# Performance work log

Hardware: AMD Instinct MI355X
Metric: run time of the kernel (lower is better)

Reference implementation:

```python
import jax, jax.numpy as jnp
import numpy as np

N_WIRES = 10
DIM = 1 << N_WIRES          # 1024 amplitudes per token state
HIDDEN = 64                 # number of Pauli-Z-string measurements (= hidden_dim)
B, T = 8, 2048

# ops[k] = Z-string on qubits in bitmask (k+1): <psi|Z_mask|psi> = sum_i |psi_i|^2 * (-1)^popcount(i & mask)
_masks = np.arange(1, HIDDEN + 1, dtype=np.int64)
_ii = np.arange(DIM, dtype=np.int64)
_pc = (((_ii[None, :] & _masks[:, None])[..., None] >> np.arange(N_WIRES)) & 1).sum(-1)
SIGNS = jnp.asarray(1.0 - 2.0 * (_pc % 2), dtype=jnp.float32)   # (HIDDEN, DIM)

CNOT = jnp.array([[1, 0, 0, 0], [0, 1, 0, 0], [0, 0, 0, 1], [0, 0, 1, 0]], dtype=jnp.complex64)

def _rx(theta):
    c = jnp.cos(theta / 2).astype(jnp.complex64)
    s = jnp.sin(theta / 2).astype(jnp.complex64)
    return jnp.stack([jnp.stack([c, -1j * s]), jnp.stack([-1j * s, c])])

def _ry(theta):
    c = jnp.cos(theta / 2).astype(jnp.complex64)
    s = jnp.sin(theta / 2).astype(jnp.complex64)
    return jnp.stack([jnp.stack([c, -s]), jnp.stack([s, c])])

def _apply_1q(psi, g, j, n):
    # qubit 0 is the most-significant bit of the state index (matches expand_operator bit order)
    left, right = 1 << j, 1 << (n - 1 - j)
    p = psi.reshape(-1, left, 2, right)
    p = jnp.einsum('ab,mlbr->mlar', g, p)
    return p.reshape(-1, 1 << n)

def _apply_2q(psi, g, q0, q1, n):
    p = psi.reshape((-1,) + (2,) * n)
    p = jnp.moveaxis(p, (1 + q0, 1 + q1), (1, 2))
    p = jnp.einsum('abcd,mcd...->mab...', g.reshape(2, 2, 2, 2), p)
    p = jnp.moveaxis(p, (1, 2), (1 + q0, 1 + q1))
    return p.reshape(-1, 1 << n)

def _forward(x, rx0, ry0, ry1):
    n, dim = N_WIRES, DIM
    Bb, Tt, C = x.shape
    M = Bb * Tt
    # AmplitudeEncoder: zero-pad features to 2^n and L2-normalize
    psi = jnp.zeros((M, dim), jnp.complex64).at[:, :C].set(x.reshape(M, C).astype(jnp.complex64))
    nrm = jnp.sqrt(jnp.sum(psi.real**2 + psi.imag**2, axis=1, keepdims=True))
    psi = psi / nrm.astype(jnp.complex64)
    # U_total = (prod_j RY1_j) (prod_j CNOT_{j,(j+1)%n}) (prod_j RY0_j RX0_j), applied to psi.
    # Applying the gate sequence directly to the state == matmul with the expanded U_total.
    rx0_d = jax.lax.stop_gradient(rx0)  # original detaches RX params via .item()
    for j in range(n):
        psi = _apply_1q(psi, _rx(rx0_d[j]), j, n)
        psi = _apply_1q(psi, _ry(ry0[j]), j, n)
    for j in range(n):
        psi = _apply_2q(psi, CNOT, j, (j + 1) % n, n)
    for j in range(n):
        psi = _apply_1q(psi, _ry(ry1[j]), j, n)
    probs = psi.real**2 + psi.imag**2            # (M, DIM)
    out = probs @ SIGNS.T                        # (M, HIDDEN) Pauli-Z-string expectations
    return out.reshape(Bb, Tt, HIDDEN).astype(jnp.float32)

def setup_inputs():
    key = jax.random.key(0)
    k1, k2, k3, k4 = jax.random.split(key, 4)
    two_pi = 2.0 * float(np.pi)
    return {
        'x': jax.random.normal(k1, (B, T, HIDDEN), dtype=jnp.float32),
        'rx0': jax.random.uniform(k2, (N_WIRES,), dtype=jnp.float32, maxval=two_pi),
        'ry0': jax.random.uniform(k3, (N_WIRES,), dtype=jnp.float32, maxval=two_pi),
        'ry1': jax.random.uniform(k4, (N_WIRES,), dtype=jnp.float32, maxval=two_pi),
    }

def reference(x, rx0, ry0, ry1):
    return _forward(x, rx0, ry0, ry1)
```

## Files before the change

kernel.cpp:

```cpp
#include <hip/hip_runtime.h>

typedef __bf16 v8bf __attribute__((ext_vector_type(8)));
typedef float v4f __attribute__((ext_vector_type(4)));
typedef unsigned short u16x8 __attribute__((ext_vector_type(8)));

__device__ __forceinline__ unsigned short f2bf(float f) {
    unsigned int u = __float_as_uint(f);
    u += 0x7FFFu + ((u >> 16) & 1u);
    return (unsigned short)(u >> 16);
}

__device__ __forceinline__ v8bf ld_bf8(const unsigned short* p) {
    u16x8 r = *(const u16x8*)p;
    return __builtin_bit_cast(v8bf, r);
}

__global__ __launch_bounds__(256) void build_V(
        const float* __restrict__ rx0, const float* __restrict__ ry0,
        const float* __restrict__ ry1,
        unsigned short* __restrict__ Vre, unsigned short* __restrict__ Vim)
{
    __shared__ float sre[1024];
    __shared__ float sim[1024];
    const int c = blockIdx.x;
    const int t = threadIdx.x;

    for (int k = 0; k < 4; ++k) {
        int i = t + k * 256;
        sre[i] = (i == c) ? 1.0f : 0.0f;
        sim[i] = 0.0f;
    }
    __syncthreads();

    for (int j = 0; j < 10; ++j) {
        float hx = 0.5f * rx0[j], hy = 0.5f * ry0[j];
        float cx = cosf(hx), sx = sinf(hx);
        float cy = cosf(hy), sy = sinf(hy);
        float g00r =  cy * cx, g00i =  sy * sx;
        float g01r = -sy * cx, g01i = -cy * sx;
        float g10r =  sy * cx, g10i = -cy * sx;
        float g11r =  cy * cx, g11i = -sy * sx;
        int p = 9 - j;
        int lowmask = (1 << p) - 1;
        #pragma unroll
        for (int it = 0; it < 2; ++it) {
            int idx = t + it * 256;
            int a = ((idx >> p) << (p + 1)) | (idx & lowmask);
            int b = a | (1 << p);
            float ar = sre[a], ai = sim[a], br = sre[b], bi = sim[b];
            sre[a] = g00r*ar - g00i*ai + g01r*br - g01i*bi;
            sim[a] = g00r*ai + g00i*ar + g01r*bi + g01i*br;
            sre[b] = g10r*ar - g10i*ai + g11r*br - g11i*bi;
            sim[b] = g10r*ai + g10i*ar + g11r*bi + g11i*br;
        }
        __syncthreads();
    }
    for (int j = 0; j < 10; ++j) {
        int pc = 9 - j;
        int pt = 9 - ((j + 1) % 10);
        int p1 = pc < pt ? pc : pt;
        int p2 = pc < pt ? pt : pc;
        int x1 = ((t >> p1) << (p1 + 1)) | (t & ((1 << p1) - 1));
        int x2 = ((x1 >> p2) << (p2 + 1)) | (x1 & ((1 << p2) - 1));
        int i0 = x2 | (1 << pc);
        int i1 = i0 | (1 << pt);
        float r0 = sre[i0], q0 = sim[i0];
        sre[i0] = sre[i1]; sim[i0] = sim[i1];
        sre[i1] = r0;      sim[i1] = q0;
        __syncthreads();
    }
    for (int j = 0; j < 10; ++j) {
        float hy = 0.5f * ry1[j];
        float cy = cosf(hy), sy = sinf(hy);
        int p = 9 - j;
        int lowmask = (1 << p) - 1;
        #pragma unroll
        for (int it = 0; it < 2; ++it) {
            int idx = t + it * 256;
            int a = ((idx >> p) << (p + 1)) | (idx & lowmask);
            int b = a | (1 << p);
            float ar = sre[a], ai = sim[a], br = sre[b], bi = sim[b];
            sre[a] = cy*ar - sy*br;  sim[a] = cy*ai - sy*bi;
            sre[b] = sy*ar + cy*br;  sim[b] = sy*ai + cy*bi;
        }
        __syncthreads();
    }
    for (int k = 0; k < 4; ++k) {
        int i = t + k * 256;
        Vre[i * 64 + c] = f2bf(sre[i]);
        Vim[i * 64 + c] = f2bf(sim[i]);
    }
}

#define LDP 72

__global__ __launch_bounds__(256) void qsa_fused(
        const float* __restrict__ x,
        const unsigned short* __restrict__ Vre,
        const unsigned short* __restrict__ Vim,
        float* __restrict__ out)
{
    __shared__ alignas(16) unsigned short xn[64][LDP];
    __shared__ alignas(16) unsigned short vre[64][LDP];
    __shared__ alignas(16) unsigned short vim[64][LDP];
    __shared__ alignas(16) unsigned short pr[64][LDP];

    const int tid = threadIdx.x;
    const int w = tid >> 6;
    const int l = tid & 63;
    const int m0 = blockIdx.x * 64;

    {
        int tok = tid >> 2, part = tid & 3;
        const float4* src = (const float4*)(x + (size_t)(m0 + tok) * 64 + part * 16);
        float4 v[4];
        float ss = 0.f;
        #pragma unroll
        for (int q = 0; q < 4; ++q) {
            v[q] = src[q];
            ss += v[q].x*v[q].x + v[q].y*v[q].y + v[q].z*v[q].z + v[q].w*v[q].w;
        }
        ss += __shfl_xor(ss, 1);
        ss += __shfl_xor(ss, 2);
        float rn = rsqrtf(ss);
        unsigned short* dst = &xn[tok][part * 16];
        #pragma unroll
        for (int q = 0; q < 4; ++q) {
            dst[q*4+0] = f2bf(v[q].x * rn);
            dst[q*4+1] = f2bf(v[q].y * rn);
            dst[q*4+2] = f2bf(v[q].z * rn);
            dst[q*4+3] = f2bf(v[q].w * rn);
        }
    }
    __syncthreads();

    const int l15 = l & 15, lh = l >> 4;

    v8bf a0 = ld_bf8(&xn[w*16 + l15][lh*8]);
    v8bf a1 = ld_bf8(&xn[w*16 + l15][32 + lh*8]);

    v4f oacc[4];
    #pragma unroll
    for (int nb = 0; nb < 4; ++nb) oacc[nb] = (v4f){0.f,0.f,0.f,0.f};

    for (int s0 = 0; s0 < 1024; s0 += 64) {
        #pragma unroll
        for (int it = 0; it < 2; ++it) {
            int idx = tid + it * 256;
            int row = idx >> 3, c8 = (idx & 7) * 8;
            *(u16x8*)&vre[row][c8] = *(const u16x8*)(Vre + (size_t)(s0 + row) * 64 + c8);
            *(u16x8*)&vim[row][c8] = *(const u16x8*)(Vim + (size_t)(s0 + row) * 64 + c8);
        }
        __syncthreads();

        v4f pre[4], pim[4];
        #pragma unroll
        for (int nb = 0; nb < 4; ++nb) {
            v8bf br0 = ld_bf8(&vre[nb*16 + l15][lh*8]);
            v8bf br1 = ld_bf8(&vre[nb*16 + l15][32 + lh*8]);
            v8bf bi0 = ld_bf8(&vim[nb*16 + l15][lh*8]);
            v8bf bi1 = ld_bf8(&vim[nb*16 + l15][32 + lh*8]);
            v4f z = (v4f){0.f,0.f,0.f,0.f};
            v4f r = __builtin_amdgcn_mfma_f32_16x16x32_bf16(a0, br0, z, 0, 0, 0);
            r     = __builtin_amdgcn_mfma_f32_16x16x32_bf16(a1, br1, r, 0, 0, 0);
            v4f q = __builtin_amdgcn_mfma_f32_16x16x32_bf16(a0, bi0, z, 0, 0, 0);
            q     = __builtin_amdgcn_mfma_f32_16x16x32_bf16(a1, bi1, q, 0, 0, 0);
            pre[nb] = r; pim[nb] = q;
        }

        #pragma unroll
        for (int nb = 0; nb < 4; ++nb) {
            #pragma unroll
            for (int r = 0; r < 4; ++r) {
                float p = pre[nb][r]*pre[nb][r] + pim[nb][r]*pim[nb][r];
                pr[w*16 + lh*4 + r][nb*16 + l15] = f2bf(p);
            }
        }

        v8bf pa0 = ld_bf8(&pr[w*16 + l15][lh*8]);
        v8bf pa1 = ld_bf8(&pr[w*16 + l15][32 + lh*8]);
        #pragma unroll
        for (int nb = 0; nb < 4; ++nb) {
            unsigned mask = (unsigned)(nb*16 + l15 + 1);
            u16x8 sA, sB;
            #pragma unroll
            for (int j = 0; j < 8; ++j) {
                int sa = s0 + lh*8 + j;
                int sb = sa + 32;
                sA[j] = (__popc(sa & mask) & 1) ? 0xBF80 : 0x3F80;
                sB[j] = (__popc(sb & mask) & 1) ? 0xBF80 : 0x3F80;
            }
            oacc[nb] = __builtin_amdgcn_mfma_f32_16x16x32_bf16(pa0, __builtin_bit_cast(v8bf, sA), oacc[nb], 0, 0, 0);
            oacc[nb] = __builtin_amdgcn_mfma_f32_16x16x32_bf16(pa1, __builtin_bit_cast(v8bf, sB), oacc[nb], 0, 0, 0);
        }
        __syncthreads();
    }

    #pragma unroll
    for (int nb = 0; nb < 4; ++nb) {
        #pragma unroll
        for (int r = 0; r < 4; ++r) {
            out[(size_t)(m0 + w*16 + lh*4 + r) * 64 + nb*16 + l15] = oacc[nb][r];
        }
    }
}

extern "C" void kernel_launch(void* const* d_in, const int* in_sizes, int n_in,
                              void* d_out, int out_size, void* d_ws, size_t ws_size,
                              hipStream_t stream) {
    const float* x   = (const float*)d_in[0];
    const float* rx0 = (const float*)d_in[1];
    const float* ry0 = (const float*)d_in[2];
    const float* ry1 = (const float*)d_in[3];
    float* out = (float*)d_out;

    unsigned short* Vre = (unsigned short*)d_ws;
    unsigned short* Vim = Vre + 1024 * 64;

    const int M = in_sizes[0] / 64;

    build_V<<<64, 256, 0, stream>>>(rx0, ry0, ry1, Vre, Vim);
    qsa_fused<<<M / 64, 256, 0, stream>>>(x, Vre, Vim, out);
}
```

Baseline: 110.7 us.

## Precompute sign matrix, split state dim across waves, read V directly from global

```diff
diff --git a/kernel.cpp b/kernel.cpp
--- a/kernel.cpp
+++ b/kernel.cpp
@@ -15,16 +15,27 @@
     return __builtin_bit_cast(v8bf, r);
 }
 
-__global__ __launch_bounds__(256) void build_V(
+__global__ __launch_bounds__(256) void build_VS(
         const float* __restrict__ rx0, const float* __restrict__ ry0,
         const float* __restrict__ ry1,
-        unsigned short* __restrict__ Vre, unsigned short* __restrict__ Vim)
+        unsigned short* __restrict__ Vre, unsigned short* __restrict__ Vim,
+        unsigned short* __restrict__ S)
 {
     __shared__ float sre[1024];
     __shared__ float sim[1024];
     const int c = blockIdx.x;
     const int t = threadIdx.x;
 
+    float cx[10], sx[10], cy0[10], sy0[10], cy1[10], sy1[10];
+    #pragma unroll
+    for (int j = 0; j < 10; ++j) {
+        float hx = 0.5f * rx0[j], h0 = 0.5f * ry0[j], h1 = 0.5f * ry1[j];
+        cx[j] = cosf(hx);  sx[j] = sinf(hx);
+        cy0[j] = cosf(h0); sy0[j] = sinf(h0);
+        cy1[j] = cosf(h1); sy1[j] = sinf(h1);
+    }
+
+    #pragma unroll
     for (int k = 0; k < 4; ++k) {
         int i = t + k * 256;
         sre[i] = (i == c) ? 1.0f : 0.0f;
@@ -33,13 +44,10 @@
     __syncthreads();
 
     for (int j = 0; j < 10; ++j) {
-        float hx = 0.5f * rx0[j], hy = 0.5f * ry0[j];
-        float cx = cosf(hx), sx = sinf(hx);
-        float cy = cosf(hy), sy = sinf(hy);
-        float g00r =  cy * cx, g00i =  sy * sx;
-        float g01r = -sy * cx, g01i = -cy * sx;
-        float g10r =  sy * cx, g10i = -cy * sx;
-        float g11r =  cy * cx, g11i = -sy * sx;
+        float g00r =  cy0[j] * cx[j], g00i =  sy0[j] * sx[j];
+        float g01r = -sy0[j] * cx[j], g01i = -cy0[j] * sx[j];
+        float g10r =  sy0[j] * cx[j], g10i = -cy0[j] * sx[j];
+        float g11r =  cy0[j] * cx[j], g11i = -sy0[j] * sx[j];
         int p = 9 - j;
         int lowmask = (1 << p) - 1;
         #pragma unroll
@@ -70,8 +78,6 @@
         __syncthreads();
     }
     for (int j = 0; j < 10; ++j) {
-        float hy = 0.5f * ry1[j];
-        float cy = cosf(hy), sy = sinf(hy);
         int p = 9 - j;
         int lowmask = (1 << p) - 1;
         #pragma unroll
@@ -80,86 +86,77 @@
             int a = ((idx >> p) << (p + 1)) | (idx & lowmask);
             int b = a | (1 << p);
             float ar = sre[a], ai = sim[a], br = sre[b], bi = sim[b];
-            sre[a] = cy*ar - sy*br;  sim[a] = cy*ai - sy*bi;
-            sre[b] = sy*ar + cy*br;  sim[b] = sy*ai + cy*bi;
+            sre[a] = cy1[j]*ar - sy1[j]*br;  sim[a] = cy1[j]*ai - sy1[j]*bi;
+            sre[b] = sy1[j]*ar + cy1[j]*br;  sim[b] = sy1[j]*ai + cy1[j]*bi;
         }
         __syncthreads();
     }
+    #pragma unroll
     for (int k = 0; k < 4; ++k) {
         int i = t + k * 256;
         Vre[i * 64 + c] = f2bf(sre[i]);
         Vim[i * 64 + c] = f2bf(sim[i]);
-    }
-}
-
-#define LDP 72
-
-__global__ __launch_bounds__(256) void qsa_fused(
+        S[c * 1024 + i] = (__popc(i & (c + 1)) & 1) ? 0xBF80 : 0x3F80;
+    }
+}
+
+__global__ __launch_bounds__(256, 2) void qsa_fused(
         const float* __restrict__ x,
         const unsigned short* __restrict__ Vre,
         const unsigned short* __restrict__ Vim,
+        const unsigned short* __restrict__ S,
         float* __restrict__ out)
 {
-    __shared__ alignas(16) unsigned short xn[64][LDP];
-    __shared__ alignas(16) unsigned short vre[64][LDP];
-    __shared__ alignas(16) unsigned short vim[64][LDP];
-    __shared__ alignas(16) unsigned short pr[64][LDP];
+    __shared__ alignas(16) unsigned short pr[4][16][72];
+    __shared__ float opart[2][16][66];
 
     const int tid = threadIdx.x;
     const int w = tid >> 6;
     const int l = tid & 63;
-    const int m0 = blockIdx.x * 64;
-
-    {
-        int tok = tid >> 2, part = tid & 3;
-        const float4* src = (const float4*)(x + (size_t)(m0 + tok) * 64 + part * 16);
-        float4 v[4];
-        float ss = 0.f;
-        #pragma unroll
-        for (int q = 0; q < 4; ++q) {
-            v[q] = src[q];
-            ss += v[q].x*v[q].x + v[q].y*v[q].y + v[q].z*v[q].z + v[q].w*v[q].w;
-        }
-        ss += __shfl_xor(ss, 1);
-        ss += __shfl_xor(ss, 2);
-        float rn = rsqrtf(ss);
-        unsigned short* dst = &xn[tok][part * 16];
-        #pragma unroll
-        for (int q = 0; q < 4; ++q) {
-            dst[q*4+0] = f2bf(v[q].x * rn);
-            dst[q*4+1] = f2bf(v[q].y * rn);
-            dst[q*4+2] = f2bf(v[q].z * rn);
-            dst[q*4+3] = f2bf(v[q].w * rn);
-        }
-    }
-    __syncthreads();
-
+    const int p = w >> 1;
+    const int h2 = w & 1;
     const int l15 = l & 15, lh = l >> 4;
-
-    v8bf a0 = ld_bf8(&xn[w*16 + l15][lh*8]);
-    v8bf a1 = ld_bf8(&xn[w*16 + l15][32 + lh*8]);
+    const int m0 = blockIdx.x * 32 + p * 16;
+
+    const float* xrow = x + (size_t)(m0 + l15) * 64;
+    float4 v0 = *(const float4*)(xrow + lh * 8);
+    float4 v1 = *(const float4*)(xrow + lh * 8 + 4);
+    float4 v2 = *(const float4*)(xrow + 32 + lh * 8);
+    float4 v3 = *(const float4*)(xrow + 32 + lh * 8 + 4);
+    float ss = v0.x*v0.x + v0.y*v0.y + v0.z*v0.z + v0.w*v0.w
+             + v1.x*v1.x + v1.y*v1.y + v1.z*v1.z + v1.w*v1.w
+             + v2.x*v2.x + v2.y*v2.y + v2.z*v2.z + v2.w*v2.w
+             + v3.x*v3.x + v3.y*v3.y + v3.z*v3.z + v3.w*v3.w;
+    ss += __shfl_xor(ss, 16);
+    ss += __shfl_xor(ss, 32);
+    float rn = rsqrtf(ss);
+    u16x8 ua0, ua1;
+    ua0[0]=f2bf(v0.x*rn); ua0[1]=f2bf(v0.y*rn); ua0[2]=f2bf(v0.z*rn); ua0[3]=f2bf(v0.w*rn);
+    ua0[4]=f2bf(v1.x*rn); ua0[5]=f2bf(v1.y*rn); ua0[6]=f2bf(v1.z*rn); ua0[7]=f2bf(v1.w*rn);
+    ua1[0]=f2bf(v2.x*rn); ua1[1]=f2bf(v2.y*rn); ua1[2]=f2bf(v2.z*rn); ua1[3]=f2bf(v2.w*rn);
+    ua1[4]=f2bf(v3.x*rn); ua1[5]=f2bf(v3.y*rn); ua1[6]=f2bf(v3.z*rn); ua1[7]=f2bf(v3.w*rn);
+    v8bf a0 = __builtin_bit_cast(v8bf, ua0);
+    v8bf a1 = __builtin_bit_cast(v8bf, ua1);
 
     v4f oacc[4];
     #pragma unroll
     for (int nb = 0; nb < 4; ++nb) oacc[nb] = (v4f){0.f,0.f,0.f,0.f};
 
-    for (int s0 = 0; s0 < 1024; s0 += 64) {
-        #pragma unroll
-        for (int it = 0; it < 2; ++it) {
-            int idx = tid + it * 256;
-            int row = idx >> 3, c8 = (idx & 7) * 8;
-            *(u16x8*)&vre[row][c8] = *(const u16x8*)(Vre + (size_t)(s0 + row) * 64 + c8);
-            *(u16x8*)&vim[row][c8] = *(const u16x8*)(Vim + (size_t)(s0 + row) * 64 + c8);
-        }
-        __syncthreads();
+    const unsigned short* vreb = Vre + (size_t)l15 * 64 + lh * 8;
+    const unsigned short* vimb = Vim + (size_t)l15 * 64 + lh * 8;
+    const unsigned short* sb   = S   + (size_t)l15 * 1024 + lh * 8;
+
+    for (int cchunk = 0; cchunk < 8; ++cchunk) {
+        const int s0 = (h2 * 8 + cchunk) * 64;
 
         v4f pre[4], pim[4];
         #pragma unroll
         for (int nb = 0; nb < 4; ++nb) {
-            v8bf br0 = ld_bf8(&vre[nb*16 + l15][lh*8]);
-            v8bf br1 = ld_bf8(&vre[nb*16 + l15][32 + lh*8]);
-            v8bf bi0 = ld_bf8(&vim[nb*16 + l15][lh*8]);
-            v8bf bi1 = ld_bf8(&vim[nb*16 + l15][32 + lh*8]);
+            const size_t ro = (size_t)(s0 + nb * 16) * 64;
+            v8bf br0 = ld_bf8(vreb + ro);
+            v8bf br1 = ld_bf8(vreb + ro + 32);
+            v8bf bi0 = ld_bf8(vimb + ro);
+            v8bf bi1 = ld_bf8(vimb + ro + 32);
             v4f z = (v4f){0.f,0.f,0.f,0.f};
             v4f r = __builtin_amdgcn_mfma_f32_16x16x32_bf16(a0, br0, z, 0, 0, 0);
             r     = __builtin_amdgcn_mfma_f32_16x16x32_bf16(a1, br1, r, 0, 0, 0);
@@ -172,36 +169,38 @@
         for (int nb = 0; nb < 4; ++nb) {
             #pragma unroll
             for (int r = 0; r < 4; ++r) {
-                float p = pre[nb][r]*pre[nb][r] + pim[nb][r]*pim[nb][r];
-                pr[w*16 + lh*4 + r][nb*16 + l15] = f2bf(p);
+                float pv = pre[nb][r]*pre[nb][r] + pim[nb][r]*pim[nb][r];
+                pr[w][lh*4 + r][nb*16 + l15] = f2bf(pv);
             }
         }
-
-        v8bf pa0 = ld_bf8(&pr[w*16 + l15][lh*8]);
-        v8bf pa1 = ld_bf8(&pr[w*16 + l15][32 + lh*8]);
+        v8bf pa0 = ld_bf8(&pr[w][l15][lh*8]);
+        v8bf pa1 = ld_bf8(&pr[w][l15][32 + lh*8]);
+
         #pragma unroll
         for (int nb = 0; nb < 4; ++nb) {
-            unsigned mask = (unsigned)(nb*16 + l15 + 1);
-            u16x8 sA, sB;
+            const size_t so = (size_t)(nb * 16) * 1024 + s0;
+            v8bf sA = ld_bf8(sb + so);
+            v8bf sB = ld_bf8(sb + so + 32);
+            oacc[nb] = __builtin_amdgcn_mfma_f32_16x16x32_bf16(pa0, sA, oacc[nb], 0, 0, 0);
+            oacc[nb] = __builtin_amdgcn_mfma_f32_16x16x32_bf16(pa1, sB, oacc[nb], 0, 0, 0);
+        }
+    }
+
+    if (h2 == 1) {
+        #pragma unroll
+        for (int nb = 0; nb < 4; ++nb)
             #pragma unroll
-            for (int j = 0; j < 8; ++j) {
-                int sa = s0 + lh*8 + j;
-                int sb = sa + 32;
-                sA[j] = (__popc(sa & mask) & 1) ? 0xBF80 : 0x3F80;
-                sB[j] = (__popc(sb & mask) & 1) ? 0xBF80 : 0x3F80;
-            }
-            oacc[nb] = __builtin_amdgcn_mfma_f32_16x16x32_bf16(pa0, __builtin_bit_cast(v8bf, sA), oacc[nb], 0, 0, 0);
-            oacc[nb] = __builtin_amdgcn_mfma_f32_16x16x32_bf16(pa1, __builtin_bit_cast(v8bf, sB), oacc[nb], 0, 0, 0);
-        }
-        __syncthreads();
-    }
-
-    #pragma unroll
-    for (int nb = 0; nb < 4; ++nb) {
-        #pragma unroll
-        for (int r = 0; r < 4; ++r) {
-            out[(size_t)(m0 + w*16 + lh*4 + r) * 64 + nb*16 + l15] = oacc[nb][r];
-        }
+            for (int r = 0; r < 4; ++r)
+                opart[p][lh*4 + r][nb*16 + l15] = oacc[nb][r];
+    }
+    __syncthreads();
+    if (h2 == 0) {
+        #pragma unroll
+        for (int nb = 0; nb < 4; ++nb)
+            #pragma unroll
+            for (int r = 0; r < 4; ++r)
+                out[(size_t)(m0 + lh*4 + r) * 64 + nb*16 + l15] =
+                    oacc[nb][r] + opart[p][lh*4 + r][nb*16 + l15];
     }
 }
 
@@ -216,9 +215,10 @@
 
     unsigned short* Vre = (unsigned short*)d_ws;
     unsigned short* Vim = Vre + 1024 * 64;
+    unsigned short* S   = Vim + 1024 * 64;
 
     const int M = in_sizes[0] / 64;
 
-    build_V<<<64, 256, 0, stream>>>(rx0, ry0, ry1, Vre, Vim);
-    qsa_fused<<<M / 64, 256, 0, stream>>>(x, Vre, Vim, out);
-}
+    build_VS<<<64, 256, 0, stream>>>(rx0, ry0, ry1, Vre, Vim, S);
+    qsa_fused<<<M / 32, 256, 0, stream>>>(x, Vre, Vim, S, out);
+}
```

Result: slower. 118.9 us (+7.4%).
